# Kernel optimization log

Hardware: AMD Instinct MI355X
Metric: run time of the kernel (lower is better)

Reference implementation:

```python
import jax, jax.numpy as jnp
import numpy as np

E = 384      # hidden_dim
H = 8        # num_attention_heads
D = E // H   # head_dim = 48


def setup_inputs() -> dict:
    key = jax.random.key(0)
    ks = jax.random.split(key, 11)
    B, S = 4, 2048
    patch_embeds = jax.random.normal(ks[0], (B, S, E), dtype=jnp.float32)
    attention_mask = jax.random.randint(ks[1], (B, S), 0, 2).astype(bool)
    s = 1.0 / np.sqrt(E)
    Wq = jax.random.normal(ks[2], (E, E), dtype=jnp.float32) * s
    bq = jnp.zeros((E,), dtype=jnp.float32)
    Wk = jax.random.normal(ks[3], (E, E), dtype=jnp.float32) * s
    bk = jnp.zeros((E,), dtype=jnp.float32)
    Wv = jax.random.normal(ks[4], (E, E), dtype=jnp.float32) * s
    bv = jnp.zeros((E,), dtype=jnp.float32)
    Wo = jax.random.normal(ks[5], (E, E), dtype=jnp.float32) * s
    bo = jnp.zeros((E,), dtype=jnp.float32)
    return {"patch_embeds": patch_embeds, "attention_mask": attention_mask,
            "Wq": Wq, "bq": bq, "Wk": Wk, "bk": bk,
            "Wv": Wv, "bv": bv, "Wo": Wo, "bo": bo}


def reference(patch_embeds, attention_mask, Wq, bq, Wk, bk, Wv, bv, Wo, bo):
    B, S, _ = patch_embeds.shape
    scale = D ** (-0.5)
    # QKV projections (nn.Linear: x @ W.T + b); W stored as [out,in]
    q = patch_embeds @ Wq.T + bq
    k = patch_embeds @ Wk.T + bk
    v = patch_embeds @ Wv.T + bv
    # [B,S,E] -> [B,H,S,D]
    q = q.reshape(B, S, H, D).transpose(0, 2, 1, 3)
    k = k.reshape(B, S, H, D).transpose(0, 2, 1, 3)
    v = v.reshape(B, S, H, D).transpose(0, 2, 1, 3)
    # scaled dot-product attention with key mask (True = masked)
    scores = jnp.einsum('bhqd,bhkd->bhqk', q, k) * scale
    mask = attention_mask[:, None, None, :]  # [B,1,1,S]
    scores = jnp.where(mask, -jnp.inf, scores)
    weights = jax.nn.softmax(scores, axis=-1)
    out = jnp.einsum('bhqk,bhkd->bhqd', weights, v)
    out = out.transpose(0, 2, 1, 3).reshape(B, S, E)
    return out @ Wo.T + bo
```

## Files before the change

kernel.cpp:

```cpp
#include <hip/hip_runtime.h>
#include <math.h>

#define B_ 4
#define S_ 2048
#define E_ 384
#define H_ 8
#define D_ 48
#define M_ (B_*S_)
#define DP_ 64
constexpr float QK_SCALE = 0.14433756729740643f * 1.4426950408889634f;

typedef __attribute__((ext_vector_type(8))) short short8;
typedef __attribute__((ext_vector_type(4))) float f32x4;
typedef unsigned short u16;

__device__ inline u16 f2bf(float f) {
    unsigned u = __float_as_uint(f);
    return (u16)((u + 0x7FFFu + ((u >> 16) & 1u)) >> 16);
}
__device__ inline float bf2f(u16 h) { return __uint_as_float(((unsigned)h) << 16); }
__device__ inline unsigned pk2(float a, float b) {
    return (unsigned)f2bf(a) | ((unsigned)f2bf(b) << 16);
}
__device__ inline unsigned pk2_fast(float a, float b) {
#if __has_builtin(__builtin_amdgcn_perm)
    unsigned ua = __float_as_uint(a) + 0x8000u;
    unsigned ub = __float_as_uint(b) + 0x8000u;
    return __builtin_amdgcn_perm(ub, ua, 0x07060302u);
#else
    return pk2(a, b);
#endif
}
__device__ inline float fexp2(float x) {
#if __has_builtin(__builtin_amdgcn_exp2f)
    return __builtin_amdgcn_exp2f(x);
#else
    return exp2f(x);
#endif
}
__device__ inline void glld16(const void* g, void* l) {
    __builtin_amdgcn_global_load_lds((const __attribute__((address_space(1))) unsigned int*)g,
                                     (__attribute__((address_space(3))) unsigned int*)l, 16, 0, 0);
}

__global__ __launch_bounds__(256) void prep(const float4* __restrict__ x,
                                            const int* __restrict__ mask,
                                            const float4* __restrict__ wq,
                                            const float4* __restrict__ wk,
                                            const float4* __restrict__ wv,
                                            const float4* __restrict__ wo,
                                            uint2* __restrict__ xb,
                                            uint2* __restrict__ wb,
                                            u16* __restrict__ Qp, u16* __restrict__ Kp) {
    const int bx = blockIdx.x, t = threadIdx.x;
    if (bx < 3072) {
        int i = bx * 256 + t;
        float4 v = x[i];
        uint2 H;
        H.x = pk2(v.x, v.y);
        H.y = pk2(v.z, v.w);
        xb[i] = H;
    } else if (bx < 3072 + 144) {
        int i = (bx - 3072) * 256 + t;
        const int n4 = 36864;
        const float4* srcs[4] = {wq, wk, wv, wo};
        #pragma unroll
        for (int j = 0; j < 4; ++j) {
            float4 v = srcs[j][i];
            uint2 H;
            H.x = pk2(v.x, v.y);
            H.y = pk2(v.z, v.w);
            wb[(size_t)j * n4 + i] = H;
        }
    } else {
        int i = (bx - 3216) * 256 + t;
        int bh = i >> 11, s = i & 2047, b = bh >> 3;
        size_t off = ((size_t)bh * S_ + s) * DP_ + 48;
        uint4 qz = {0x00004300u, 0, 0, 0};
        uint4 kz = {mask[b * S_ + s] ? 0x0000BF80u : 0u, 0, 0, 0};
        uint4 z  = {0, 0, 0, 0};
        *reinterpret_cast<uint4*>(Qp + off)     = qz;
        *reinterpret_cast<uint4*>(Qp + off + 8) = z;
        *reinterpret_cast<uint4*>(Kp + off)     = kz;
        *reinterpret_cast<uint4*>(Kp + off + 8) = z;
    }
}

template <int MT>
__device__ __forceinline__ void gemm_core(const u16* __restrict__ ab,
                                          const u16* __restrict__ wbp,
                                          int m0, int n0, f32x4 acc[MT][4],
                                          u16* As, u16* Ws) {
    const int t = threadIdx.x, w = t >> 6, lane = t & 63;
    const int ln = lane & 15, quad = lane >> 4;
    const int gr = lane >> 3;
    const int gc = (lane & 7) ^ gr;

    #pragma unroll
    for (int mt = 0; mt < MT; ++mt)
        #pragma unroll
        for (int nt = 0; nt < 4; ++nt)
            acc[mt][nt] = (f32x4){0.f, 0.f, 0.f, 0.f};

    auto stage = [&](int bf, int kk) {
        u16* Ab = As + bf * (MT * 4096);
        u16* Wb = Ws + bf * 4096;
        #pragma unroll
        for (int i = 0; i < 2 * MT; ++i) {
            int r0 = w * (16 * MT) + i * 8;
            glld16(ab + (size_t)(m0 + r0 + gr) * E_ + kk + gc * 8, Ab + r0 * 64);
        }
        #pragma unroll
        for (int i = 0; i < 2; ++i) {
            int r0 = w * 16 + i * 8;
            glld16(wbp + (size_t)(n0 + r0 + gr) * E_ + kk + gc * 8, Wb + r0 * 64);
        }
    };

    stage(0, 0);
    __syncthreads();

    #pragma unroll
    for (int it = 0; it < 6; ++it) {
        const int cur = it & 1;
        if (it < 5) stage(cur ^ 1, (it + 1) * 64);
        const u16* Ab = As + cur * (MT * 4096);
        const u16* Wb = Ws + cur * 4096;
        #pragma unroll
        for (int ks = 0; ks < 2; ++ks) {
            const int slot = (ks * 4 + quad) ^ (ln & 7);
            short8 ah[MT], wfh[4];
            #pragma unroll
            for (int mt = 0; mt < MT; ++mt) {
                int row = w * (16 * MT) + mt * 16 + ln;
                ah[mt] = *reinterpret_cast<const short8*>(&Ab[row * 64 + slot * 8]);
            }
            #pragma unroll
            for (int nt = 0; nt < 4; ++nt) {
                int row = nt * 16 + ln;
                wfh[nt] = *reinterpret_cast<const short8*>(&Wb[row * 64 + slot * 8]);
            }
            #pragma unroll
            for (int mt = 0; mt < MT; ++mt)
                #pragma unroll
                for (int nt = 0; nt < 4; ++nt)
                    acc[mt][nt] = __builtin_amdgcn_mfma_f32_16x16x32_bf16(ah[mt], wfh[nt], acc[mt][nt], 0, 0, 0);
        }
        __syncthreads();
    }
}

__global__ __launch_bounds__(256) void gemm_qkv(const u16* __restrict__ xb,
                                                const u16* __restrict__ wb,
                                                const float* __restrict__ bq, const float* __restrict__ bk,
                                                const float* __restrict__ bv,
                                                u16* __restrict__ Qp, u16* __restrict__ Kp,
                                                u16* __restrict__ Vtp) {
    __shared__ u16 smem[2 * 2 * 4096 + 2 * 4096];
    u16* As = smem;
    u16* Ws = smem + 2 * 2 * 4096;

    const int y = blockIdx.y;
    const int wsel = y / 6;
    const int n0 = (y - wsel * 6) * 64;
    const int m0 = blockIdx.x * 128;
    const u16* wh = wb + (size_t)wsel * 147456;

    f32x4 acc[2][4];
    gemm_core<2>(xb, wh, m0, n0, acc, As, Ws);

    const int t = threadIdx.x, w = t >> 6, lane = t & 63;
    const int ln = lane & 15, quad = lane >> 4;
    const int b  = m0 >> 11;
    const float* bias = (wsel == 0) ? bq : (wsel == 1) ? bk : bv;

    if (wsel == 2) {
        const int s_base = (m0 & 2047) + w * 32 + quad * 4;
        #pragma unroll
        for (int nt = 0; nt < 4; ++nt) {
            const int col = n0 + nt * 16 + ln;
            const int h   = (col * 683) >> 15;
            const int d   = col - h * 48;
            const float bc = bias[col];
            u16* dst = Vtp + ((size_t)(b * 8 + h) * 48 + d) * 2048;
            #pragma unroll
            for (int mt = 0; mt < 2; ++mt) {
                int s0 = s_base + mt * 16;
                uint2 pk;
                pk.x = pk2(acc[mt][nt][0] + bc, acc[mt][nt][1] + bc);
                pk.y = pk2(acc[mt][nt][2] + bc, acc[mt][nt][3] + bc);
                *reinterpret_cast<uint2*>(dst + s0) = pk;
            }
        }
    } else {
        const float scale = (wsel == 0) ? QK_SCALE : 1.0f;
        u16* Tr = smem;
        __syncthreads();
        #pragma unroll
        for (int nt = 0; nt < 4; ++nt) {
            const float bc = bias[n0 + nt * 16 + ln];
            #pragma unroll
            for (int mt = 0; mt < 2; ++mt)
                #pragma unroll
                for (int r = 0; r < 4; ++r) {
                    int row = w * 32 + mt * 16 + quad * 4 + r;
                    Tr[row * 76 + nt * 16 + ln] = f2bf((acc[mt][nt][r] + bc) * scale);
                }
        }
        __syncthreads();
        const int row  = t >> 1, half = t & 1;
        const int s    = (m0 & 2047) + row;
        const u16* src = &Tr[row * 76 + half * 32];
        u16* base = (wsel == 0) ? Qp : Kp;
        #pragma unroll
        for (int c = 0; c < 4; ++c) {
            int gcol = n0 + half * 32 + c * 8;
            int h = (gcol * 683) >> 15;
            int d = gcol - h * 48;
            u16* dst = base + ((size_t)(b * 8 + h) * 2048 + s) * DP_ + d;
            *reinterpret_cast<uint4*>(dst) = *reinterpret_cast<const uint4*>(src + c * 8);
        }
    }
}

__global__ __launch_bounds__(256) void gemm_out(const u16* __restrict__ ab,
                                                const u16* __restrict__ wb,
                                                const float* __restrict__ bo, float* __restrict__ out) {
    __shared__ u16 smem[2 * 4096 + 2 * 4096];
    u16* As = smem;
    u16* Ws = smem + 2 * 4096;
    const int m0 = blockIdx.x * 64, n0 = blockIdx.y * 64;
    const u16* wh = wb + (size_t)3 * 147456;
    f32x4 acc[1][4];
    gemm_core<1>(ab, wh, m0, n0, acc, As, Ws);

    const int t = threadIdx.x, w = t >> 6, lane = t & 63;
    const int ln = lane & 15, quad = lane >> 4;
    #pragma unroll
    for (int nt = 0; nt < 4; ++nt) {
        const int col = n0 + nt * 16 + ln;
        const float bc = bo[col];
        #pragma unroll
        for (int r = 0; r < 4; ++r) {
            size_t row = (size_t)(m0 + w * 16 + quad * 4 + r);
            out[row * E_ + col] = acc[0][nt][r] + bc;
        }
    }
}

__global__ __launch_bounds__(256, 2) void attn_mfma(const u16* __restrict__ Qp,
                                                    const u16* __restrict__ Kp,
                                                    const u16* __restrict__ Vtp,
                                                    u16* __restrict__ AO) {
    __shared__ __align__(16) u16 QPs[128 * 64];
    __shared__ __align__(16) u16 Ksh[2][64 * 64];
    __shared__ __align__(16) u16 Vt[2][48 * 64];
    __shared__ float linv[4][32];

    const int t    = threadIdx.x;
    const int w    = t >> 6;
    const int lane = t & 63;
    const int ln   = lane & 15;
    const int quad = lane >> 4;
    const int gr   = lane >> 3;
    const int gc   = (lane & 7) ^ gr;
    const int bh   = blockIdx.x;
    const int q0   = blockIdx.y * 128;
    const int b    = bh >> 3, h = bh & 7;
    const int cb   = h * 48;
    const size_t rb = (size_t)b * S_;

    const u16* Qsrc = Qp  + ((size_t)bh * S_ + q0) * DP_;
    const u16* Ksrc = Kp  + (size_t)bh * S_ * DP_;
    const u16* Vsrc = Vtp + (size_t)bh * 48 * 2048;

    const int swz0 = ((quad    ) ^ (ln & 7)) << 3;
    const int swz1 = ((4 + quad) ^ (ln & 7)) << 3;
    const u16* kA[2][2], *vA[2][2];
    #pragma unroll
    for (int bf = 0; bf < 2; ++bf) {
        kA[bf][0] = &Ksh[bf][ln * 64 + swz0];
        kA[bf][1] = &Ksh[bf][ln * 64 + swz1];
        vA[bf][0] = &Vt[bf][ln * 64 + swz0];
        vA[bf][1] = &Vt[bf][ln * 64 + swz1];
    }
    int qrow[2];
    const u16 *pR[2][2];
    u16* pW[2][4];
    #pragma unroll
    for (int qt = 0; qt < 2; ++qt) {
        qrow[qt] = (w * 32 + qt * 16 + ln) * 64;
        pR[qt][0] = &QPs[qrow[qt] + swz0];
        pR[qt][1] = &QPs[qrow[qt] + swz1];
        #pragma unroll
        for (int Mt = 0; Mt < 4; ++Mt)
            pW[qt][Mt] = &QPs[qrow[qt] +
                ((((Mt * 2 + (quad >> 1)) ^ (ln & 7)) << 3) | ((quad & 1) << 2))];
    }

    auto stage = [&](int bf, int kt) {
        const int k0 = kt * 64;
        glld16(Ksrc + (size_t)(k0 + w * 16 + gr) * DP_ + gc * 8,     &Ksh[bf][(w * 16) * 64]);
        glld16(Ksrc + (size_t)(k0 + w * 16 + 8 + gr) * DP_ + gc * 8, &Ksh[bf][(w * 16 + 8) * 64]);
        if (w < 3) {
            glld16(Vsrc + (size_t)(w * 16 + gr) * 2048 + k0 + gc * 8,     &Vt[bf][(w * 16) * 64]);
            glld16(Vsrc + (size_t)(w * 16 + 8 + gr) * 2048 + k0 + gc * 8, &Vt[bf][(w * 16 + 8) * 64]);
        }
    };

    #pragma unroll
    for (int i = 0; i < 4; ++i) {
        int r0 = w * 32 + i * 8;
        glld16(Qsrc + (size_t)(r0 + gr) * DP_ + gc * 8, &QPs[r0 * 64]);
    }
    stage(0, 0);
    __syncthreads();

    short8 qf[2][2];
    #pragma unroll
    for (int qt = 0; qt < 2; ++qt) {
        qf[qt][0] = *reinterpret_cast<const short8*>(pR[qt][0]);
        qf[qt][1] = *reinterpret_cast<const short8*>(pR[qt][1]);
    }

    f32x4 o[2][3];
    #pragma unroll
    for (int qt = 0; qt < 2; ++qt)
        #pragma unroll
        for (int nt = 0; nt < 3; ++nt) o[qt][nt] = (f32x4){0.f, 0.f, 0.f, 0.f};
    float lq[2] = {0.f, 0.f};

    auto body = [&](int cur, int nxt, int ktn) {
        if (ktn < 32) stage(nxt, ktn);

        f32x4 sc[4][2];
        #pragma unroll
        for (int Mt = 0; Mt < 4; ++Mt) {
            short8 kf0 = *reinterpret_cast<const short8*>(kA[cur][0] + Mt * 1024);
            short8 kf1 = *reinterpret_cast<const short8*>(kA[cur][1] + Mt * 1024);
            #pragma unroll
            for (int qt = 0; qt < 2; ++qt) {
                f32x4 a0 = __builtin_amdgcn_mfma_f32_16x16x32_bf16(kf0, qf[qt][0], (f32x4){0.f,0.f,0.f,0.f}, 0, 0, 0);
                sc[Mt][qt] = __builtin_amdgcn_mfma_f32_16x16x32_bf16(kf1, qf[qt][1], a0, 0, 0, 0);
            }
        }

        #pragma unroll
        for (int qt = 0; qt < 2; ++qt)
            #pragma unroll
            for (int Mt = 0; Mt < 4; ++Mt) {
                float p0 = fexp2(sc[Mt][qt][0]);
                float p1 = fexp2(sc[Mt][qt][1]);
                float p2 = fexp2(sc[Mt][qt][2]);
                float p3 = fexp2(sc[Mt][qt][3]);
                lq[qt] += (p0 + p1) + (p2 + p3);
                uint2 pk;
                pk.x = pk2_fast(p0, p1);
                pk.y = pk2_fast(p2, p3);
                *reinterpret_cast<uint2*>(pW[qt][Mt]) = pk;
            }

        short8 pa[2][2];
        #pragma unroll
        for (int qt = 0; qt < 2; ++qt) {
            pa[qt][0] = *reinterpret_cast<const short8*>(pR[qt][0]);
            pa[qt][1] = *reinterpret_cast<const short8*>(pR[qt][1]);
        }
        #pragma unroll
        for (int nt = 0; nt < 3; ++nt) {
            short8 vb0 = *reinterpret_cast<const short8*>(vA[cur][0] + nt * 1024);
            short8 vb1 = *reinterpret_cast<const short8*>(vA[cur][1] + nt * 1024);
            #pragma unroll
            for (int qt = 0; qt < 2; ++qt) {
                o[qt][nt] = __builtin_amdgcn_mfma_f32_16x16x32_bf16(pa[qt][0], vb0, o[qt][nt], 0, 0, 0);
                o[qt][nt] = __builtin_amdgcn_mfma_f32_16x16x32_bf16(pa[qt][1], vb1, o[qt][nt], 0, 0, 0);
            }
        }
        __syncthreads();
    };

    for (int kt = 0; kt < 32; kt += 2) {
        body(0, 1, kt + 1);
        body(1, 0, kt + 2);
    }

    #pragma unroll
    for (int qt = 0; qt < 2; ++qt) {
        float l = lq[qt];
        l += __shfl_xor(l, 16);
        l += __shfl_xor(l, 32);
        if (quad == 0) linv[w][qt * 16 + ln] = 1.0f / l;
    }
    __syncthreads();
    #pragma unroll
    for (int qt = 0; qt < 2; ++qt) {
        f32x4 il = *reinterpret_cast<const f32x4*>(&linv[w][qt * 16 + quad * 4]);
        #pragma unroll
        for (int nt = 0; nt < 3; ++nt)
            #pragma unroll
            for (int r = 0; r < 4; ++r) {
                size_t row = rb + q0 + w * 32 + qt * 16 + quad * 4 + r;
                size_t idx = row * E_ + cb + nt * 16 + ln;
                AO[idx] = f2bf(o[qt][nt][r] * il[r]);
            }
    }
}

extern "C" void kernel_launch(void* const* d_in, const int* in_sizes, int n_in,
                              void* d_out, int out_size, void* d_ws, size_t ws_size,
                              hipStream_t stream) {
    (void)in_sizes; (void)n_in; (void)out_size; (void)ws_size;
    const float* x    = (const float*)d_in[0];
    const int*   mask = (const int*)  d_in[1];
    const float* Wq   = (const float*)d_in[2];
    const float* bq   = (const float*)d_in[3];
    const float* Wk   = (const float*)d_in[4];
    const float* bk   = (const float*)d_in[5];
    const float* Wv   = (const float*)d_in[6];
    const float* bv   = (const float*)d_in[7];
    const float* Wo   = (const float*)d_in[8];
    const float* bo   = (const float*)d_in[9];

    const size_t NELEM = (size_t)M_ * E_;
    const size_t WELEM = (size_t)E_ * E_;
    const size_t PEL   = (size_t)B_ * H_ * S_ * DP_;
    u16* ws = (u16*)d_ws;
    u16* xb  = ws;
    u16* wb  = xb + NELEM;
    u16* Qp  = wb + 4 * WELEM;
    u16* Kp  = Qp + PEL;
    u16* Vtp = Kp + PEL;
    u16* AO  = xb;

    dim3 blk(256);
    prep<<<dim3(3472), blk, 0, stream>>>(
        (const float4*)x, mask,
        (const float4*)Wq, (const float4*)Wk, (const float4*)Wv, (const float4*)Wo,
        (uint2*)xb, (uint2*)wb, Qp, Kp);

    gemm_qkv<<<dim3(M_ / 128, 18), blk, 0, stream>>>(xb, wb, bq, bk, bv, Qp, Kp, Vtp);

    attn_mfma<<<dim3(B_ * H_, S_ / 128), blk, 0, stream>>>(Qp, Kp, Vtp, AO);

    gemm_out<<<dim3(M_ / 64, 6), blk, 0, stream>>>(AO, wb, bo, (float*)d_out);
}
```

Before: 148.3 us.

## Fuse Q/K/V projections into one GEMM sharing the activation tile

Replaces the QKV GEMM, which used a grid of 18 column blocks with one weight matrix each, with a kernel where each block computes the Q, K and V outputs for a 64-row tile. The activation tile is loaded into shared memory once and reused across all three weight matrices, which cuts redundant activation reads. The new kernel drops double-buffering and instead uses a synchronous load-then-compute loop per k-step, so global-load latency is no longer overlapped. It also inlines the GEMM core into gemm_out without changing that kernel's behaviour.

```diff
diff --git a/kernel.cpp b/kernel.cpp
--- a/kernel.cpp
+++ b/kernel.cpp
@@ -86,139 +86,108 @@
     }
 }
 
-template <int MT>
-__device__ __forceinline__ void gemm_core(const u16* __restrict__ ab,
-                                          const u16* __restrict__ wbp,
-                                          int m0, int n0, f32x4 acc[MT][4],
-                                          u16* As, u16* Ws) {
+__global__ __launch_bounds__(256) void gemm_qkv3(const u16* __restrict__ xb,
+                                                 const u16* __restrict__ wb,
+                                                 const float* __restrict__ bq,
+                                                 const float* __restrict__ bk,
+                                                 const float* __restrict__ bv,
+                                                 u16* __restrict__ Qp, u16* __restrict__ Kp,
+                                                 u16* __restrict__ Vtp) {
+    __shared__ u16 smem[4 * 4096];
+    u16* As = smem;
+
     const int t = threadIdx.x, w = t >> 6, lane = t & 63;
     const int ln = lane & 15, quad = lane >> 4;
     const int gr = lane >> 3;
     const int gc = (lane & 7) ^ gr;
-
-    #pragma unroll
-    for (int mt = 0; mt < MT; ++mt)
+    const int m0 = blockIdx.x * 64;
+    const int n0 = blockIdx.y * 64;
+    const int b  = m0 >> 11;
+
+    f32x4 acc[3][4];
+    #pragma unroll
+    for (int j = 0; j < 3; ++j)
         #pragma unroll
         for (int nt = 0; nt < 4; ++nt)
-            acc[mt][nt] = (f32x4){0.f, 0.f, 0.f, 0.f};
-
-    auto stage = [&](int bf, int kk) {
-        u16* Ab = As + bf * (MT * 4096);
-        u16* Wb = Ws + bf * 4096;
-        #pragma unroll
-        for (int i = 0; i < 2 * MT; ++i) {
-            int r0 = w * (16 * MT) + i * 8;
-            glld16(ab + (size_t)(m0 + r0 + gr) * E_ + kk + gc * 8, Ab + r0 * 64);
-        }
+            acc[j][nt] = (f32x4){0.f, 0.f, 0.f, 0.f};
+
+    for (int kk = 0; kk < 384; kk += 64) {
+        __syncthreads();
         #pragma unroll
         for (int i = 0; i < 2; ++i) {
             int r0 = w * 16 + i * 8;
-            glld16(wbp + (size_t)(n0 + r0 + gr) * E_ + kk + gc * 8, Wb + r0 * 64);
-        }
-    };
-
-    stage(0, 0);
-    __syncthreads();
-
-    #pragma unroll
-    for (int it = 0; it < 6; ++it) {
-        const int cur = it & 1;
-        if (it < 5) stage(cur ^ 1, (it + 1) * 64);
-        const u16* Ab = As + cur * (MT * 4096);
-        const u16* Wb = Ws + cur * 4096;
+            glld16(xb + (size_t)(m0 + r0 + gr) * E_ + kk + gc * 8, As + r0 * 64);
+        }
+        #pragma unroll
+        for (int j = 0; j < 3; ++j)
+            #pragma unroll
+            for (int i = 0; i < 2; ++i) {
+                int r0 = w * 16 + i * 8;
+                glld16(wb + (size_t)j * 147456 + (size_t)(n0 + r0 + gr) * E_ + kk + gc * 8,
+                       smem + (1 + j) * 4096 + r0 * 64);
+            }
+        __syncthreads();
+
         #pragma unroll
         for (int ks = 0; ks < 2; ++ks) {
             const int slot = (ks * 4 + quad) ^ (ln & 7);
-            short8 ah[MT], wfh[4];
-            #pragma unroll
-            for (int mt = 0; mt < MT; ++mt) {
-                int row = w * (16 * MT) + mt * 16 + ln;
-                ah[mt] = *reinterpret_cast<const short8*>(&Ab[row * 64 + slot * 8]);
-            }
-            #pragma unroll
-            for (int nt = 0; nt < 4; ++nt) {
-                int row = nt * 16 + ln;
-                wfh[nt] = *reinterpret_cast<const short8*>(&Wb[row * 64 + slot * 8]);
-            }
-            #pragma unroll
-            for (int mt = 0; mt < MT; ++mt)
+            short8 ah = *reinterpret_cast<const short8*>(&As[(w * 16 + ln) * 64 + slot * 8]);
+            #pragma unroll
+            for (int j = 0; j < 3; ++j) {
+                const u16* Wsj = smem + (1 + j) * 4096;
                 #pragma unroll
-                for (int nt = 0; nt < 4; ++nt)
-                    acc[mt][nt] = __builtin_amdgcn_mfma_f32_16x16x32_bf16(ah[mt], wfh[nt], acc[mt][nt], 0, 0, 0);
-        }
-        __syncthreads();
-    }
-}
-
-__global__ __launch_bounds__(256) void gemm_qkv(const u16* __restrict__ xb,
-                                                const u16* __restrict__ wb,
-                                                const float* __restrict__ bq, const float* __restrict__ bk,
-                                                const float* __restrict__ bv,
-                                                u16* __restrict__ Qp, u16* __restrict__ Kp,
-                                                u16* __restrict__ Vtp) {
-    __shared__ u16 smem[2 * 2 * 4096 + 2 * 4096];
-    u16* As = smem;
-    u16* Ws = smem + 2 * 2 * 4096;
-
-    const int y = blockIdx.y;
-    const int wsel = y / 6;
-    const int n0 = (y - wsel * 6) * 64;
-    const int m0 = blockIdx.x * 128;
-    const u16* wh = wb + (size_t)wsel * 147456;
-
-    f32x4 acc[2][4];
-    gemm_core<2>(xb, wh, m0, n0, acc, As, Ws);
-
-    const int t = threadIdx.x, w = t >> 6, lane = t & 63;
-    const int ln = lane & 15, quad = lane >> 4;
-    const int b  = m0 >> 11;
-    const float* bias = (wsel == 0) ? bq : (wsel == 1) ? bk : bv;
-
-    if (wsel == 2) {
-        const int s_base = (m0 & 2047) + w * 32 + quad * 4;
+                for (int nt = 0; nt < 4; ++nt) {
+                    short8 wf = *reinterpret_cast<const short8*>(&Wsj[(nt * 16 + ln) * 64 + slot * 8]);
+                    acc[j][nt] = __builtin_amdgcn_mfma_f32_16x16x32_bf16(ah, wf, acc[j][nt], 0, 0, 0);
+                }
+            }
+        }
+    }
+
+    {
+        const int s_base = (m0 & 2047) + w * 16 + quad * 4;
         #pragma unroll
         for (int nt = 0; nt < 4; ++nt) {
             const int col = n0 + nt * 16 + ln;
             const int h   = (col * 683) >> 15;
             const int d   = col - h * 48;
-            const float bc = bias[col];
+            const float bc = bv[col];
             u16* dst = Vtp + ((size_t)(b * 8 + h) * 48 + d) * 2048;
-            #pragma unroll
-            for (int mt = 0; mt < 2; ++mt) {
-                int s0 = s_base + mt * 16;
-                uint2 pk;
-                pk.x = pk2(acc[mt][nt][0] + bc, acc[mt][nt][1] + bc);
-                pk.y = pk2(acc[mt][nt][2] + bc, acc[mt][nt][3] + bc);
-                *reinterpret_cast<uint2*>(dst + s0) = pk;
-            }
-        }
-    } else {
-        const float scale = (wsel == 0) ? QK_SCALE : 1.0f;
-        u16* Tr = smem;
-        __syncthreads();
-        #pragma unroll
-        for (int nt = 0; nt < 4; ++nt) {
-            const float bc = bias[n0 + nt * 16 + ln];
-            #pragma unroll
-            for (int mt = 0; mt < 2; ++mt)
-                #pragma unroll
-                for (int r = 0; r < 4; ++r) {
-                    int row = w * 32 + mt * 16 + quad * 4 + r;
-                    Tr[row * 76 + nt * 16 + ln] = f2bf((acc[mt][nt][r] + bc) * scale);
-                }
-        }
-        __syncthreads();
-        const int row  = t >> 1, half = t & 1;
-        const int s    = (m0 & 2047) + row;
-        const u16* src = &Tr[row * 76 + half * 32];
-        u16* base = (wsel == 0) ? Qp : Kp;
-        #pragma unroll
-        for (int c = 0; c < 4; ++c) {
-            int gcol = n0 + half * 32 + c * 8;
+            uint2 pk;
+            pk.x = pk2(acc[2][nt][0] + bc, acc[2][nt][1] + bc);
+            pk.y = pk2(acc[2][nt][2] + bc, acc[2][nt][3] + bc);
+            *reinterpret_cast<uint2*>(dst + s_base) = pk;
+        }
+    }
+
+    u16* TrQ = smem;
+    u16* TrK = smem + 64 * 76;
+    __syncthreads();
+    #pragma unroll
+    for (int nt = 0; nt < 4; ++nt) {
+        const int col = n0 + nt * 16 + ln;
+        const float bcq = bq[col], bck = bk[col];
+        #pragma unroll
+        for (int r = 0; r < 4; ++r) {
+            int row = w * 16 + quad * 4 + r;
+            TrQ[row * 76 + nt * 16 + ln] = f2bf((acc[0][nt][r] + bcq) * QK_SCALE);
+            TrK[row * 76 + nt * 16 + ln] = f2bf(acc[1][nt][r] + bck);
+        }
+    }
+    __syncthreads();
+    {
+        const int row = t >> 2, quarter = t & 3;
+        const int s   = (m0 & 2047) + row;
+        #pragma unroll
+        for (int c = 0; c < 2; ++c) {
+            int gcol = n0 + quarter * 16 + c * 8;
             int h = (gcol * 683) >> 15;
             int d = gcol - h * 48;
-            u16* dst = base + ((size_t)(b * 8 + h) * 2048 + s) * DP_ + d;
-            *reinterpret_cast<uint4*>(dst) = *reinterpret_cast<const uint4*>(src + c * 8);
+            size_t off = ((size_t)(b * 8 + h) * 2048 + s) * DP_ + d;
+            *reinterpret_cast<uint4*>(Qp + off) =
+                *reinterpret_cast<const uint4*>(&TrQ[row * 76 + quarter * 16 + c * 8]);
+            *reinterpret_cast<uint4*>(Kp + off) =
+                *reinterpret_cast<const uint4*>(&TrK[row * 76 + quarter * 16 + c * 8]);
         }
     }
 }
@@ -229,13 +198,47 @@
     __shared__ u16 smem[2 * 4096 + 2 * 4096];
     u16* As = smem;
     u16* Ws = smem + 2 * 4096;
+    const int t = threadIdx.x, w = t >> 6, lane = t & 63;
+    const int ln = lane & 15, quad = lane >> 4;
+    const int gr = lane >> 3;
+    const int gc = (lane & 7) ^ gr;
     const int m0 = blockIdx.x * 64, n0 = blockIdx.y * 64;
     const u16* wh = wb + (size_t)3 * 147456;
-    f32x4 acc[1][4];
-    gemm_core<1>(ab, wh, m0, n0, acc, As, Ws);
-
-    const int t = threadIdx.x, w = t >> 6, lane = t & 63;
-    const int ln = lane & 15, quad = lane >> 4;
+
+    f32x4 acc[4];
+    #pragma unroll
+    for (int nt = 0; nt < 4; ++nt) acc[nt] = (f32x4){0.f, 0.f, 0.f, 0.f};
+
+    auto stage = [&](int bf, int kk) {
+        #pragma unroll
+        for (int i = 0; i < 2; ++i) {
+            int r0 = w * 16 + i * 8;
+            glld16(ab + (size_t)(m0 + r0 + gr) * E_ + kk + gc * 8, As + bf * 4096 + r0 * 64);
+            glld16(wh + (size_t)(n0 + r0 + gr) * E_ + kk + gc * 8, Ws + bf * 4096 + r0 * 64);
+        }
+    };
+
+    stage(0, 0);
+    __syncthreads();
+    #pragma unroll
+    for (int it = 0; it < 6; ++it) {
+        const int cur = it & 1;
+        if (it < 5) stage(cur ^ 1, (it + 1) * 64);
+        const u16* Ab = As + cur * 4096;
+        const u16* Wb = Ws + cur * 4096;
+        #pragma unroll
+        for (int ks = 0; ks < 2; ++ks) {
+            const int slot = (ks * 4 + quad) ^ (ln & 7);
+            short8 ah = *reinterpret_cast<const short8*>(&Ab[(w * 16 + ln) * 64 + slot * 8]);
+            #pragma unroll
+            for (int nt = 0; nt < 4; ++nt) {
+                short8 wf = *reinterpret_cast<const short8*>(&Wb[(nt * 16 + ln) * 64 + slot * 8]);
+                acc[nt] = __builtin_amdgcn_mfma_f32_16x16x32_bf16(ah, wf, acc[nt], 0, 0, 0);
+            }
+        }
+        __syncthreads();
+    }
+
     #pragma unroll
     for (int nt = 0; nt < 4; ++nt) {
         const int col = n0 + nt * 16 + ln;
@@ -243,7 +246,7 @@
         #pragma unroll
         for (int r = 0; r < 4; ++r) {
             size_t row = (size_t)(m0 + w * 16 + quad * 4 + r);
-            out[row * E_ + col] = acc[0][nt][r] + bc;
+            out[row * E_ + col] = acc[nt][r] + bc;
         }
     }
 }
@@ -438,7 +441,7 @@
         (const float4*)Wq, (const float4*)Wk, (const float4*)Wv, (const float4*)Wo,
         (uint2*)xb, (uint2*)wb, Qp, Kp);
 
-    gemm_qkv<<<dim3(M_ / 128, 18), blk, 0, stream>>>(xb, wb, bq, bk, bv, Qp, Kp, Vtp);
+    gemm_qkv3<<<dim3(M_ / 64, 6), blk, 0, stream>>>(xb, wb, bq, bk, bv, Qp, Kp, Vtp);
 
     attn_mfma<<<dim3(B_ * H_, S_ / 128), blk, 0, stream>>>(Qp, Kp, Vtp, AO);
 
```

After: 147.5 us. About the same (-0.5%).
